# Kernel tuning notes

Measured on AMD Instinct MI355X. Metric: run time of the kernel, lower is better.

Reference implementation:

```python
import jax, jax.numpy as jnp
import numpy as np

NUM_GRAPHS = 8
NEG_SLOPE = 0.2


def add_self_loops(edge_index, n):
    loops = jnp.arange(n, dtype=edge_index.dtype)
    src = jnp.concatenate([edge_index[0], loops])
    dst = jnp.concatenate([edge_index[1], loops])
    return src, dst


def gat_conv(x, src, dst, W, att_src, att_dst, bias, concat):
    # x: [N, F_in]; W: [F_in, H*C]; att_src/att_dst: [H, C]; bias: [H*C] or [C]
    n = x.shape[0]
    H, C = att_src.shape
    xl = (x @ W).reshape(n, H, C)                     # [N, H, C]
    a_src = jnp.einsum('nhc,hc->nh', xl, att_src)     # [N, H]
    a_dst = jnp.einsum('nhc,hc->nh', xl, att_dst)     # [N, H]
    e = jax.nn.leaky_relu(a_src[src] + a_dst[dst], NEG_SLOPE)  # [E, H]
    # segment softmax over edges grouped by destination node
    m = jax.ops.segment_max(e, dst, num_segments=n)   # [N, H]
    e = jnp.exp(e - m[dst])
    denom = jax.ops.segment_sum(e, dst, num_segments=n)
    alpha = e / (denom[dst] + 1e-16)                  # [E, H]
    msg = xl[src] * alpha[:, :, None]                 # [E, H, C]
    out = jax.ops.segment_sum(msg, dst, num_segments=n)  # [N, H, C]
    out = out.reshape(n, H * C) if concat else out.mean(axis=1)
    return out + bias


def global_mean_pool(x, batch, num_graphs):
    s = jax.ops.segment_sum(x, batch, num_segments=num_graphs)
    cnt = jax.ops.segment_sum(jnp.ones((x.shape[0],), x.dtype), batch, num_segments=num_graphs)
    return s / jnp.maximum(cnt, 1.0)[:, None]


def setup_inputs() -> dict:
    key = jax.random.key(0)
    ks = jax.random.split(key, 12)
    N, E, F_in, Ch, H, F_out = 50000, 800000, 128, 64, 4, 128
    x = jax.random.normal(ks[0], (N, F_in), dtype=jnp.float32)
    edge_index = jax.random.randint(ks[1], (2, E), 0, N, dtype=jnp.int64)
    batch = jnp.sort(jax.random.randint(ks[2], (N,), 0, NUM_GRAPHS, dtype=jnp.int64))
    s = 0.1
    W1 = jax.random.normal(ks[3], (F_in, H * Ch), dtype=jnp.float32) * s
    att_src1 = jax.random.normal(ks[4], (H, Ch), dtype=jnp.float32) * s
    att_dst1 = jax.random.normal(ks[5], (H, Ch), dtype=jnp.float32) * s
    bias1 = jnp.zeros((H * Ch,), dtype=jnp.float32)
    W2 = jax.random.normal(ks[6], (H * Ch, F_out), dtype=jnp.float32) * s
    att_src2 = jax.random.normal(ks[7], (1, F_out), dtype=jnp.float32) * s
    att_dst2 = jax.random.normal(ks[8], (1, F_out), dtype=jnp.float32) * s
    bias2 = jnp.zeros((F_out,), dtype=jnp.float32)
    return {"x": x, "edge_index": edge_index, "batch": batch,
            "W1": W1, "att_src1": att_src1, "att_dst1": att_dst1, "bias1": bias1,
            "W2": W2, "att_src2": att_src2, "att_dst2": att_dst2, "bias2": bias2}


def reference(x, edge_index, batch, W1, att_src1, att_dst1, bias1, W2, att_src2, att_dst2, bias2):
    n = x.shape[0]
    src, dst = add_self_loops(edge_index, n)
    h = gat_conv(x, src, dst, W1, att_src1, att_dst1, bias1, concat=True)
    h = jax.nn.relu(h)
    h = gat_conv(h, src, dst, W2, att_src2, att_dst2, bias2, concat=False)
    return global_mean_pool(h, batch, NUM_GRAPHS)
```

## Files before the change

kernel.cpp:

```cpp
#include <hip/hip_runtime.h>
#include <cstdint>
#include <cstddef>

#define NEG_SLOPE 0.2f
#define LOG2E 1.44269504088896f

typedef __attribute__((ext_vector_type(8))) short bf16x8;
typedef __attribute__((ext_vector_type(4))) float f32x4;
typedef __attribute__((ext_vector_type(2))) float f32x2;

__device__ __forceinline__ ushort f2b(float f) {
  unsigned u = __float_as_uint(f);
  return (ushort)((u + 0x7FFFu + ((u >> 16) & 1)) >> 16);
}
__device__ __forceinline__ float fexp2(float x) {
#if __has_builtin(__builtin_amdgcn_exp2f)
  return __builtin_amdgcn_exp2f(x);
#else
  return __exp2f(x);
#endif
}
__device__ __forceinline__ int lbound(const int* __restrict__ a, int n, int key) {
  int lo = 0, hi = n;
  while (lo < hi) { int m = (lo + hi) >> 1; if (a[m] < key) lo = m + 1; else hi = m; }
  return lo;
}

__global__ __launch_bounds__(256) void pack_w_both(const float* __restrict__ W1,
                                                   ushort* __restrict__ Bp1,
                                                   const float* __restrict__ W2,
                                                   ushort* __restrict__ Bp2) {
  int i = blockIdx.x * 256 + threadIdx.x;
  if (i >= 128 * 256) return;
  {
    int k = i >> 8, n = i & 255;
    Bp1[(((size_t)(k >> 3) * 256 + n) << 3) + (k & 7)] = f2b(W1[i]);
  }
  {
    int k = i >> 7, n = i & 127;
    Bp2[(((size_t)(k >> 3) * 128 + n) << 3) + (k & 7)] = f2b(W2[i]);
  }
}

template<int N, int K, int C, int H, bool AF32>
__global__ __launch_bounds__(256) void gemm_attn(const void* __restrict__ A_,
                                                 const ushort* __restrict__ Bp,
                                                 const float* __restrict__ att_src,
                                                 const float* __restrict__ att_dst,
                                                 unsigned char* __restrict__ C8,
                                                 float* __restrict__ a_src,
                                                 float* __restrict__ a_dst, int M) {
  const int wave = threadIdx.x >> 6;
  const int lane = threadIdx.x & 63;
  const int strips = M / 16;
  const int strip = blockIdx.x * 4 + wave;
  if (strip >= strips) return;
  const int r = lane & 15, kg = lane >> 4;
  const int row = strip * 16 + r;

  bf16x8 a[K / 32];
  if constexpr (AF32) {
    const float* Af = (const float*)A_;
    #pragma unroll
    for (int k0 = 0; k0 < K / 32; ++k0) {
      float4 f0 = *(const float4*)(Af + (size_t)row * K + k0 * 32 + kg * 8);
      float4 f1 = *(const float4*)(Af + (size_t)row * K + k0 * 32 + kg * 8 + 4);
      bf16x8 t;
      t[0] = (short)f2b(f0.x); t[1] = (short)f2b(f0.y);
      t[2] = (short)f2b(f0.z); t[3] = (short)f2b(f0.w);
      t[4] = (short)f2b(f1.x); t[5] = (short)f2b(f1.y);
      t[6] = (short)f2b(f1.z); t[7] = (short)f2b(f1.w);
      a[k0] = t;
    }
  } else {
    const ushort* Ab = (const ushort*)A_;
    #pragma unroll
    for (int k0 = 0; k0 < K / 32; ++k0)
      a[k0] = *(const bf16x8*)(Ab + (size_t)row * K + k0 * 32 + kg * 8);
  }

  float as_part[4] = {}, ad_part[4] = {};
  #pragma unroll 2
  for (int n0 = 0; n0 < N / 16; ++n0) {
    f32x4 acc = {0.f, 0.f, 0.f, 0.f};
    #pragma unroll
    for (int k0 = 0; k0 < K / 32; ++k0) {
      bf16x8 b = *(const bf16x8*)(Bp + ((size_t)(k0 * 4 + kg) * N + n0 * 16 + r) * 8);
      acc = __builtin_amdgcn_mfma_f32_16x16x32_bf16(a[k0], b, acc, 0, 0, 0);
    }
    float asv = att_src[n0 * 16 + r] * LOG2E;
    float adv = att_dst[n0 * 16 + r] * LOG2E;
    #pragma unroll
    for (int i = 0; i < 4; ++i) {
      as_part[i] = fmaf(acc[i], asv, as_part[i]);
      ad_part[i] = fmaf(acc[i], adv, ad_part[i]);
    }
    #pragma unroll
    for (int i = 0; i < 4; ++i) {
      int pk = __builtin_amdgcn_cvt_pk_fp8_f32(acc[i], acc[i], 0, false);
      C8[((size_t)strip * 16 + kg * 4 + i) * N + n0 * 16 + r] = (unsigned char)(pk & 0xFF);
    }
    if (((n0 + 1) * 16) % C == 0) {
      int h = (n0 * 16) / C;
      #pragma unroll
      for (int i = 0; i < 4; ++i) {
        float ts = as_part[i], td = ad_part[i];
        #pragma unroll
        for (int off = 1; off < 16; off <<= 1) {
          ts += __shfl_xor(ts, off);
          td += __shfl_xor(td, off);
        }
        if (r == i) {
          a_src[(size_t)(strip * 16 + kg * 4 + i) * H + h] = ts;
          a_dst[(size_t)(strip * 16 + kg * 4 + i) * H + h] = td;
        }
        as_part[i] = 0.f;
        ad_part[i] = 0.f;
      }
    }
  }
}

__global__ __launch_bounds__(256) void rank_k(const int* __restrict__ edst,
                                              int* __restrict__ hist,
                                              int* __restrict__ rank, int E) {
  int e = blockIdx.x * 256 + threadIdx.x;
  if (e >= E) return;
  rank[e] = atomicAdd(hist + edst[e], 1);
}

__global__ __launch_bounds__(256) void scan1_k(const int* __restrict__ hist,
                                               int* __restrict__ excl,
                                               int* __restrict__ chunksum, int n) {
  __shared__ int sums[256];
  int base = blockIdx.x * 1024 + threadIdx.x * 4;
  int4 v = {0, 0, 0, 0};
  if (base + 3 < n) v = *(const int4*)(hist + base);
  else {
    if (base < n)     v.x = hist[base];
    if (base + 1 < n) v.y = hist[base + 1];
    if (base + 2 < n) v.z = hist[base + 2];
    if (base + 3 < n) v.w = hist[base + 3];
  }
  int s = v.x + v.y + v.z + v.w;
  sums[threadIdx.x] = s;
  __syncthreads();
  for (int off = 1; off < 256; off <<= 1) {
    int t = (threadIdx.x >= (unsigned)off) ? sums[threadIdx.x - off] : 0;
    __syncthreads();
    sums[threadIdx.x] += t;
    __syncthreads();
  }
  if (threadIdx.x == 255) chunksum[blockIdx.x] = sums[255];
  int e0 = sums[threadIdx.x] - s;
  int e1 = e0 + v.x, e2 = e1 + v.y, e3 = e2 + v.z;
  if (base + 3 < n) {
    int4 o = {e0, e1, e2, e3};
    *(int4*)(excl + base) = o;
  } else {
    if (base < n)     excl[base] = e0;
    if (base + 1 < n) excl[base + 1] = e1;
    if (base + 2 < n) excl[base + 2] = e2;
    if (base + 3 < n) excl[base + 3] = e3;
  }
}

__global__ void scan2_k(const int* __restrict__ chunksum,
                        int* __restrict__ chunkoff, int nchunks) {
  if (threadIdx.x == 0) {
    int run = 0;
    for (int c = 0; c < nchunks; ++c) { chunkoff[c] = run; run += chunksum[c]; }
  }
}

__global__ __launch_bounds__(256) void addoff_k(int* __restrict__ rowptr,
                                                const int* __restrict__ chunkoff,
                                                int n, int total) {
  int i = blockIdx.x * 256 + threadIdx.x;
  if (i == 0) rowptr[n] = total;
  if (i >= n) return;
  rowptr[i] += chunkoff[i >> 10];
}

__global__ __launch_bounds__(256) void fill_k(const int* __restrict__ esrc,
                                              const int* __restrict__ edst,
                                              const int* __restrict__ rowptr,
                                              const int* __restrict__ rank,
                                              int* __restrict__ csr_src, int E) {
  int e = blockIdx.x * 256 + threadIdx.x;
  if (e >= E) return;
  csr_src[rowptr[edst[e]] + rank[e]] = esrc[e];
}

template<int H, int C>
__global__ __launch_bounds__(256) void agg1_k(const int* __restrict__ rowptr,
                                              const int* __restrict__ csr,
                                              const float* __restrict__ a_src,
                                              const float* __restrict__ a_dst,
                                              const unsigned char* __restrict__ xl,
                                              const float* __restrict__ bias,
                                              ushort* __restrict__ out, int n) {
  constexpr int F = H * C;
  constexpr int PER = F / 64;
  constexpr int U = 8;
  const int wid = (blockIdx.x * 256 + threadIdx.x) >> 6;
  const int lane = threadIdx.x & 63;
  if (wid >= n) return;
  const int h = lane / (64 / H);
  const uint lofs = (uint)lane * PER;
  const int beg = rowptr[wid];
  const int end = rowptr[wid + 1];
  const float adh = a_dst[(uint)wid * H + h];

  float vs = a_src[(uint)wid * H + h] + adh;
  vs = fmaxf(vs, NEG_SLOPE * vs);
  float den = 1.f;
  float acc[PER];
  {
    uint xs = *(const uint*)(xl + ((uint)wid * F + lofs));
    f32x2 lo = __builtin_amdgcn_cvt_pk_f32_fp8(xs, false);
    f32x2 hi = __builtin_amdgcn_cvt_pk_f32_fp8(xs, true);
    acc[0] = lo[0]; acc[1] = lo[1]; acc[2] = hi[0]; acc[3] = hi[1];
  }

  for (int j = beg; j < end; j += U) {
    int s[U];
    #pragma unroll
    for (int u = 0; u < U; ++u) s[u] = csr[j + u];
    uint xv[U];
    #pragma unroll
    for (int u = 0; u < U; ++u)
      xv[u] = *(const uint*)(xl + ((uint)s[u] * F + lofs));
    float p[U];
    #pragma unroll
    for (int u = 0; u < U; ++u) {
      float t = a_src[(uint)s[u] * H + h] + adh;
      t = fmaxf(t, NEG_SLOPE * t);
      t = (j + u < end) ? t - vs : -1e30f;
      p[u] = fexp2(t);
    }
    float ps = 0.f;
    #pragma unroll
    for (int u = 0; u < U; ++u) ps += p[u];
    den += ps;
    #pragma unroll
    for (int u = 0; u < U; ++u) {
      f32x2 lo = __builtin_amdgcn_cvt_pk_f32_fp8(xv[u], false);
      f32x2 hi = __builtin_amdgcn_cvt_pk_f32_fp8(xv[u], true);
      acc[0] = fmaf(p[u], lo[0], acc[0]);
      acc[1] = fmaf(p[u], lo[1], acc[1]);
      acc[2] = fmaf(p[u], hi[0], acc[2]);
      acc[3] = fmaf(p[u], hi[1], acc[3]);
    }
  }

  float inv = 1.f / (den + 1e-16f);
  float o[PER];
  #pragma unroll
  for (int i = 0; i < PER; ++i)
    o[i] = fmaxf(fmaf(acc[i], inv, bias[lane * PER + i]), 0.f);
  ushort4 ov = {f2b(o[0]), f2b(o[1]), f2b(o[2]), f2b(o[3])};
  *(ushort4*)(out + (size_t)wid * F + lane * PER) = ov;
}

__global__ __launch_bounds__(256) void agg2_k(const int* __restrict__ rowptr,
                                              const int* __restrict__ csr,
                                              const float* __restrict__ a_src,
                                              const float* __restrict__ a_dst,
                                              const unsigned char* __restrict__ xl,
                                              float* __restrict__ out2,
                                              int n, int Emax) {
  constexpr int U = 8;
  const int pair = (blockIdx.x * 256 + threadIdx.x) >> 6;
  const int lane = threadIdx.x & 63;
  const int l32 = lane & 31;
  int wid = pair * 2 + (lane >> 5);
  const bool act = wid < n;
  if (!act) wid = n - 1;
  const uint lofs = (uint)l32 * 4;
  const int beg = rowptr[wid];
  const int deg = rowptr[wid + 1] - beg;
  const int mdeg = max(deg, __shfl_xor(deg, 32));
  const float adh = a_dst[wid];

  float vs = a_src[wid] + adh;
  vs = fmaxf(vs, NEG_SLOPE * vs);
  float den = 1.f;
  float acc[4];
  {
    uint xs = *(const uint*)(xl + ((uint)wid * 128 + lofs));
    f32x2 lo = __builtin_amdgcn_cvt_pk_f32_fp8(xs, false);
    f32x2 hi = __builtin_amdgcn_cvt_pk_f32_fp8(xs, true);
    acc[0] = lo[0]; acc[1] = lo[1]; acc[2] = hi[0]; acc[3] = hi[1];
  }

  for (int j = 0; j < mdeg; j += U) {
    int s[U];
    #pragma unroll
    for (int u = 0; u < U; ++u) s[u] = csr[min(beg + j + u, Emax)];
    uint xv[U];
    #pragma unroll
    for (int u = 0; u < U; ++u)
      xv[u] = *(const uint*)(xl + ((uint)s[u] * 128 + lofs));
    float p[U];
    #pragma unroll
    for (int u = 0; u < U; ++u) {
      float t = a_src[s[u]] + adh;
      t = fmaxf(t, NEG_SLOPE * t);
      t = (j + u < deg) ? t - vs : -1e30f;
      p[u] = fexp2(t);
    }
    float ps = 0.f;
    #pragma unroll
    for (int u = 0; u < U; ++u) ps += p[u];
    den += ps;
    #pragma unroll
    for (int u = 0; u < U; ++u) {
      f32x2 lo = __builtin_amdgcn_cvt_pk_f32_fp8(xv[u], false);
      f32x2 hi = __builtin_amdgcn_cvt_pk_f32_fp8(xv[u], true);
      acc[0] = fmaf(p[u], lo[0], acc[0]);
      acc[1] = fmaf(p[u], lo[1], acc[1]);
      acc[2] = fmaf(p[u], hi[0], acc[2]);
      acc[3] = fmaf(p[u], hi[1], acc[3]);
    }
  }

  if (act) {
    float inv = 1.f / (den + 1e-16f);
    float4 ov = {acc[0] * inv, acc[1] * inv, acc[2] * inv, acc[3] * inv};
    *(float4*)(out2 + (size_t)wid * 128 + l32 * 4) = ov;
  }
}

__global__ __launch_bounds__(256) void pool2_k(const float* __restrict__ out2,
                                               const int* __restrict__ batch,
                                               float* __restrict__ pp, int n) {
  const int g = blockIdx.y;
  const int b = blockIdx.x;
  const int lo = lbound(batch, n, g);
  const int hi = lbound(batch, n, g + 1);
  const int cnt = hi - lo;
  const int span = (cnt + 31) >> 5;
  const int s0 = lo + b * span;
  const int s1 = min(s0 + span, hi);
  const int qid = threadIdx.x & 31;
  const int phase = threadIdx.x >> 5;

  float4 a = {0.f, 0.f, 0.f, 0.f};
  for (int node = s0 + phase; node < s1; node += 8) {
    float4 v = *(const float4*)(out2 + (size_t)node * 128 + qid * 4);
    a.x += v.x; a.y += v.y; a.z += v.z; a.w += v.w;
  }
  __shared__ float red[8][128];
  *(float4*)&red[phase][qid * 4] = a;
  __syncthreads();
  if (threadIdx.x < 128) {
    float s = 0.f;
    #pragma unroll
    for (int ph = 0; ph < 8; ++ph) s += red[ph][threadIdx.x];
    pp[((size_t)g * 32 + b) * 128 + threadIdx.x] = s;
  }
}

__global__ __launch_bounds__(256) void finalize_k(const float* __restrict__ pp,
                                                  const int* __restrict__ batch,
                                                  const float* __restrict__ bias2,
                                                  float* __restrict__ out, int n) {
  int t = blockIdx.x * 256 + threadIdx.x;
  if (t >= 8 * 128) return;
  int g = t >> 7, c = t & 127;
  float s = 0.f;
  #pragma unroll
  for (int b = 0; b < 32; ++b) s += pp[((size_t)g * 32 + b) * 128 + c];
  int lo = lbound(batch, n, g);
  int hi = lbound(batch, n, g + 1);
  float cnt = (float)(hi - lo);
  out[t] = s / fmaxf(cnt, 1.f) + bias2[c];
}

extern "C" void kernel_launch(void* const* d_in, const int* in_sizes, int n_in,
                              void* d_out, int out_size, void* d_ws, size_t ws_size,
                              hipStream_t stream) {
  const float* x        = (const float*)d_in[0];
  const int*   ei       = (const int*)d_in[1];
  const int*   batch    = (const int*)d_in[2];
  const float* W1       = (const float*)d_in[3];
  const float* att_src1 = (const float*)d_in[4];
  const float* att_dst1 = (const float*)d_in[5];
  const float* bias1    = (const float*)d_in[6];
  const float* W2       = (const float*)d_in[7];
  const float* att_src2 = (const float*)d_in[8];
  const float* att_dst2 = (const float*)d_in[9];
  const float* bias2    = (const float*)d_in[10];
  float* out = (float*)d_out;

  const int E  = in_sizes[1] / 2;
  const int NN = in_sizes[2];
  const int* esrc = ei;
  const int* edst = ei + E;
  const int PAD = 64;

  char* w = (char*)d_ws;
  size_t woff = 0;
  auto walloc = [&](size_t bytes) -> char* {
    char* r = w + woff;
    woff += (bytes + 255) & ~(size_t)255;
    return r;
  };
  unsigned char* xl1 = (unsigned char*)walloc((size_t)NN * 256);
  ushort* h1     = (ushort*)walloc((size_t)NN * 256 * 2);
  unsigned char* xl2 = (unsigned char*)walloc((size_t)NN * 128);
  float*  a_src1 = (float*)walloc((size_t)NN * 4 * 4);
  float*  a_dst1 = (float*)walloc((size_t)NN * 4 * 4);
  float*  a_src2 = (float*)walloc((size_t)NN * 4);
  float*  a_dst2 = (float*)walloc((size_t)NN * 4);
  int*    rowptr = (int*)walloc((size_t)(NN + 1) * 4);
  int*    hist   = (int*)walloc((size_t)NN * 4);
  int*    rank   = (int*)walloc((size_t)E * 4);
  int*    csrsrc = (int*)walloc((size_t)(E + PAD) * 4);
  ushort* Bp1    = (ushort*)walloc(128 * 256 * 2);
  ushort* Bp2    = (ushort*)walloc(256 * 128 * 2);
  int*    chunks = (int*)walloc(256 * 4);
  int*    chunko = (int*)walloc(256 * 4);
  float*  pp     = (float*)walloc(8 * 32 * 128 * 4);
  float*  out2   = (float*)h1;

  dim3 blk(256);
  const int nbE = (E + 255) / 256;
  const int nbN4 = (NN + 3) / 4;
  const int nbP  = ((NN + 1) / 2 + 3) / 4;
  const int nchunks = (NN + 1023) / 1024;
  const int gblocks = (NN / 16 + 3) / 4;

  hipMemsetAsync(hist, 0, (size_t)NN * 4, stream);
  hipMemsetAsync(csrsrc + E, 0, PAD * 4, stream);
  rank_k<<<nbE, blk, 0, stream>>>(edst, hist, rank, E);
  scan1_k<<<nchunks, blk, 0, stream>>>(hist, rowptr, chunks, NN);
  scan2_k<<<1, 64, 0, stream>>>(chunks, chunko, nchunks);
  addoff_k<<<(NN + 255) / 256, blk, 0, stream>>>(rowptr, chunko, NN, E);
  fill_k<<<nbE, blk, 0, stream>>>(esrc, edst, rowptr, rank, csrsrc, E);

  pack_w_both<<<(128 * 256 + 255) / 256, blk, 0, stream>>>(W1, Bp1, W2, Bp2);

  gemm_attn<256, 128, 64, 4, true><<<gblocks, blk, 0, stream>>>(
      x, Bp1, att_src1, att_dst1, xl1, a_src1, a_dst1, NN);
  agg1_k<4, 64><<<nbN4, blk, 0, stream>>>(
      rowptr, csrsrc, a_src1, a_dst1, xl1, bias1, h1, NN);

  gemm_attn<128, 256, 128, 1, false><<<gblocks, blk, 0, stream>>>(
      h1, Bp2, att_src2, att_dst2, xl2, a_src2, a_dst2, NN);
  agg2_k<<<nbP, blk, 0, stream>>>(
      rowptr, csrsrc, a_src2, a_dst2, xl2, out2, NN, E + PAD - 1);

  {
    dim3 grid2(32, 8);
    pool2_k<<<grid2, blk, 0, stream>>>(out2, batch, pp, NN);
  }
  finalize_k<<<4, blk, 0, stream>>>(pp, batch, bias2, out, NN);
}
```

Measured before the change: 193.0 us.

## Compute edge attention weights cooperatively across lanes and broadcast via shuffles

In both aggregation kernels each lane now loads one edge's source index and attention logit, computes its exponent once, and broadcasts weights (and in agg2 the source indices) to the other lanes with shuffles. Before, every lane loaded all neighbor indices and logits and computed all exponentials itself. The unroll grows to 16 edges per step, and the padding memset is folded into the fill kernel. This cuts redundant scalar loads and exp work per edge, at the cost of extra cross-lane shuffles, more registers, and larger padded tails for low-degree nodes.

```diff
diff --git a/kernel.cpp b/kernel.cpp
--- a/kernel.cpp
+++ b/kernel.cpp
@@ -186,10 +186,11 @@
                                               const int* __restrict__ edst,
                                               const int* __restrict__ rowptr,
                                               const int* __restrict__ rank,
-                                              int* __restrict__ csr_src, int E) {
+                                              int* __restrict__ csr_src,
+                                              int E, int Epad) {
   int e = blockIdx.x * 256 + threadIdx.x;
-  if (e >= E) return;
-  csr_src[rowptr[edst[e]] + rank[e]] = esrc[e];
+  if (e < E) csr_src[rowptr[edst[e]] + rank[e]] = esrc[e];
+  else if (e < Epad) csr_src[e] = 0;
 }
 
 template<int H, int C>
@@ -201,21 +202,23 @@
                                               const float* __restrict__ bias,
                                               ushort* __restrict__ out, int n) {
   constexpr int F = H * C;
-  constexpr int PER = F / 64;
-  constexpr int U = 8;
-  const int wid = (blockIdx.x * 256 + threadIdx.x) >> 6;
+  const int wid0 = (blockIdx.x * 256 + threadIdx.x) >> 6;
+  if (wid0 >= n) return;
+  const int wid = __builtin_amdgcn_readfirstlane(wid0);
   const int lane = threadIdx.x & 63;
-  if (wid >= n) return;
-  const int h = lane / (64 / H);
-  const uint lofs = (uint)lane * PER;
+  const int h = lane >> 4;
+  const uint lofs = (uint)lane * 4;
+  const int j4 = lane & 3;
+  const int je = lane >> 2;
   const int beg = rowptr[wid];
   const int end = rowptr[wid + 1];
-  const float adh = a_dst[(uint)wid * H + h];
-
-  float vs = a_src[(uint)wid * H + h] + adh;
-  vs = fmaxf(vs, NEG_SLOPE * vs);
+
+  const float adh_s = a_dst[(uint)wid * 4 + j4];
+  float vs_s = a_src[(uint)wid * 4 + j4] + adh_s;
+  vs_s = fmaxf(vs_s, NEG_SLOPE * vs_s);
+
   float den = 1.f;
-  float acc[PER];
+  float acc[4];
   {
     uint xs = *(const uint*)(xl + ((uint)wid * F + lofs));
     f32x2 lo = __builtin_amdgcn_cvt_pk_f32_fp8(xs, false);
@@ -223,44 +226,38 @@
     acc[0] = lo[0]; acc[1] = lo[1]; acc[2] = hi[0]; acc[3] = hi[1];
   }
 
-  for (int j = beg; j < end; j += U) {
-    int s[U];
-    #pragma unroll
-    for (int u = 0; u < U; ++u) s[u] = csr[j + u];
-    uint xv[U];
-    #pragma unroll
-    for (int u = 0; u < U; ++u)
-      xv[u] = *(const uint*)(xl + ((uint)s[u] * F + lofs));
-    float p[U];
-    #pragma unroll
-    for (int u = 0; u < U; ++u) {
-      float t = a_src[(uint)s[u] * H + h] + adh;
-      t = fmaxf(t, NEG_SLOPE * t);
-      t = (j + u < end) ? t - vs : -1e30f;
-      p[u] = fexp2(t);
-    }
-    float ps = 0.f;
-    #pragma unroll
-    for (int u = 0; u < U; ++u) ps += p[u];
-    den += ps;
-    #pragma unroll
-    for (int u = 0; u < U; ++u) {
+  for (int j = beg; j < end; j += 16) {
+    int sl = csr[j + je];
+    float t = a_src[(uint)sl * 4 + j4] + adh_s;
+    t = fmaxf(t, NEG_SLOPE * t);
+    t = (j + je < end) ? t - vs_s : -1e30f;
+    float pl = fexp2(t);
+    uint xv[16];
+    #pragma unroll
+    for (int u = 0; u < 16; ++u) {
+      int su = csr[j + u];
+      xv[u] = *(const uint*)(xl + ((uint)su * F + lofs));
+    }
+    #pragma unroll
+    for (int u = 0; u < 16; ++u) {
+      float pu = __shfl(pl, u * 4 + h);
+      den += pu;
       f32x2 lo = __builtin_amdgcn_cvt_pk_f32_fp8(xv[u], false);
       f32x2 hi = __builtin_amdgcn_cvt_pk_f32_fp8(xv[u], true);
-      acc[0] = fmaf(p[u], lo[0], acc[0]);
-      acc[1] = fmaf(p[u], lo[1], acc[1]);
-      acc[2] = fmaf(p[u], hi[0], acc[2]);
-      acc[3] = fmaf(p[u], hi[1], acc[3]);
+      acc[0] = fmaf(pu, lo[0], acc[0]);
+      acc[1] = fmaf(pu, lo[1], acc[1]);
+      acc[2] = fmaf(pu, hi[0], acc[2]);
+      acc[3] = fmaf(pu, hi[1], acc[3]);
     }
   }
 
   float inv = 1.f / (den + 1e-16f);
-  float o[PER];
+  float o[4];
   #pragma unroll
-  for (int i = 0; i < PER; ++i)
-    o[i] = fmaxf(fmaf(acc[i], inv, bias[lane * PER + i]), 0.f);
+  for (int i = 0; i < 4; ++i)
+    o[i] = fmaxf(fmaf(acc[i], inv, bias[lane * 4 + i]), 0.f);
   ushort4 ov = {f2b(o[0]), f2b(o[1]), f2b(o[2]), f2b(o[3])};
-  *(ushort4*)(out + (size_t)wid * F + lane * PER) = ov;
+  *(ushort4*)(out + (size_t)wid * F + lane * 4) = ov;
 }
 
 __global__ __launch_bounds__(256) void agg2_k(const int* __restrict__ rowptr,
@@ -270,11 +267,11 @@
                                               const unsigned char* __restrict__ xl,
                                               float* __restrict__ out2,
                                               int n, int Emax) {
-  constexpr int U = 8;
   const int pair = (blockIdx.x * 256 + threadIdx.x) >> 6;
   const int lane = threadIdx.x & 63;
   const int l32 = lane & 31;
-  int wid = pair * 2 + (lane >> 5);
+  const int half = lane >> 5;
+  int wid = pair * 2 + half;
   const bool act = wid < n;
   if (!act) wid = n - 1;
   const uint lofs = (uint)l32 * 4;
@@ -294,34 +291,32 @@
     acc[0] = lo[0]; acc[1] = lo[1]; acc[2] = hi[0]; acc[3] = hi[1];
   }
 
-  for (int j = 0; j < mdeg; j += U) {
-    int s[U];
-    #pragma unroll
-    for (int u = 0; u < U; ++u) s[u] = csr[min(beg + j + u, Emax)];
-    uint xv[U];
-    #pragma unroll
-    for (int u = 0; u < U; ++u)
-      xv[u] = *(const uint*)(xl + ((uint)s[u] * 128 + lofs));
-    float p[U];
-    #pragma unroll
-    for (int u = 0; u < U; ++u) {
-      float t = a_src[s[u]] + adh;
-      t = fmaxf(t, NEG_SLOPE * t);
-      t = (j + u < deg) ? t - vs : -1e30f;
-      p[u] = fexp2(t);
-    }
-    float ps = 0.f;
-    #pragma unroll
-    for (int u = 0; u < U; ++u) ps += p[u];
-    den += ps;
-    #pragma unroll
-    for (int u = 0; u < U; ++u) {
-      f32x2 lo = __builtin_amdgcn_cvt_pk_f32_fp8(xv[u], false);
-      f32x2 hi = __builtin_amdgcn_cvt_pk_f32_fp8(xv[u], true);
-      acc[0] = fmaf(p[u], lo[0], acc[0]);
-      acc[1] = fmaf(p[u], lo[1], acc[1]);
-      acc[2] = fmaf(p[u], hi[0], acc[2]);
-      acc[3] = fmaf(p[u], hi[1], acc[3]);
+  for (int j = 0; j < mdeg; j += 32) {
+    int sl = csr[min(beg + j + l32, Emax)];
+    float t = a_src[sl] + adh;
+    t = fmaxf(t, NEG_SLOPE * t);
+    t = (j + l32 < deg) ? t - vs : -1e30f;
+    float pl = fexp2(t);
+    #pragma unroll
+    for (int g = 0; g < 2; ++g) {
+      int su[16];
+      uint xv[16];
+      #pragma unroll
+      for (int u = 0; u < 16; ++u) {
+        su[u] = __shfl(sl, half * 32 + g * 16 + u);
+        xv[u] = *(const uint*)(xl + ((uint)su[u] * 128 + lofs));
+      }
+      #pragma unroll
+      for (int u = 0; u < 16; ++u) {
+        float pu = __shfl(pl, half * 32 + g * 16 + u);
+        den += pu;
+        f32x2 lo = __builtin_amdgcn_cvt_pk_f32_fp8(xv[u], false);
+        f32x2 hi = __builtin_amdgcn_cvt_pk_f32_fp8(xv[u], true);
+        acc[0] = fmaf(pu, lo[0], acc[0]);
+        acc[1] = fmaf(pu, lo[1], acc[1]);
+        acc[2] = fmaf(pu, hi[0], acc[2]);
+        acc[3] = fmaf(pu, hi[1], acc[3]);
+      }
     }
   }
 
@@ -426,19 +421,19 @@
   float*  out2   = (float*)h1;
 
   dim3 blk(256);
-  const int nbE = (E + 255) / 256;
+  const int nbE  = (E + 255) / 256;
+  const int nbEp = (E + PAD + 255) / 256;
   const int nbN4 = (NN + 3) / 4;
   const int nbP  = ((NN + 1) / 2 + 3) / 4;
   const int nchunks = (NN + 1023) / 1024;
   const int gblocks = (NN / 16 + 3) / 4;
 
   hipMemsetAsync(hist, 0, (size_t)NN * 4, stream);
-  hipMemsetAsync(csrsrc + E, 0, PAD * 4, stream);
   rank_k<<<nbE, blk, 0, stream>>>(edst, hist, rank, E);
   scan1_k<<<nchunks, blk, 0, stream>>>(hist, rowptr, chunks, NN);
   scan2_k<<<1, 64, 0, stream>>>(chunks, chunko, nchunks);
   addoff_k<<<(NN + 255) / 256, blk, 0, stream>>>(rowptr, chunko, NN, E);
-  fill_k<<<nbE, blk, 0, stream>>>(esrc, edst, rowptr, rank, csrsrc, E);
+  fill_k<<<nbEp, blk, 0, stream>>>(esrc, edst, rowptr, rank, csrsrc, E, E + PAD);
 
   pack_w_both<<<(128 * 256 + 255) / 256, blk, 0, stream>>>(W1, Bp1, W2, Bp2);
 
```

New measurement: 188.9 us. 2.1% less time.
